# Kernel optimization log

Measured on AMD Instinct MI355X. Metric: run time of the kernel, lower is better.

Reference implementation:

```python
import jax, jax.numpy as jnp
import numpy as np

B, TE, TD, H, N_HIDDEN = 8, 4096, 1024, 256, 256

def setup_inputs() -> dict:
    key = jax.random.key(0)
    k_e, k_d, k_w, k_b = jax.random.split(key, 4)
    e = jax.random.normal(k_e, (B, TE, H), dtype=jnp.float32)
    d = jax.random.normal(k_d, (B, TD, H), dtype=jnp.float32)
    # Dense(n_hidden, activation='tanh') params: kernel [2H, n_hidden], bias [n_hidden]
    W = jax.random.normal(k_w, (2 * H, N_HIDDEN), dtype=jnp.float32) * (1.0 / np.sqrt(2 * H))
    b = jnp.zeros((N_HIDDEN,), dtype=jnp.float32)
    return {"e": e, "d": d, "W": W, "b": b}

def reference(e, d, W, b):
    # scores: Dot(axes=(2,2)) -> [B, Td, Te]
    scores = jnp.einsum('bth,bsh->bts', d, e)
    attn = jax.nn.softmax(scores, axis=-1)
    # value: Dot(axes=(2,1)) -> [B, Td, H]
    value = jnp.einsum('bts,bsh->bth', attn, e)
    concat = jnp.concatenate([value, d], axis=-1)  # [B, Td, 2H]
    return jnp.tanh(concat @ W + b)  # [B, Td, n_hidden]
```

## Files before the change

kernel.cpp:

```cpp
#include <hip/hip_runtime.h>


#define B_ 8
#define TE_ 4096
#define TD_ 1024
#define H_ 256
#define NS_ 4
#define CHUNK_ (TE_ / NS_)
#define NIT_ (CHUNK_ / 32)
#define NROW_ (B_ * TD_)

typedef __attribute__((ext_vector_type(8))) short s16x8;
typedef __attribute__((ext_vector_type(8))) _Float16 h16x8;
typedef __attribute__((ext_vector_type(4))) float fx4;
typedef __attribute__((ext_vector_type(16))) float fx16;
typedef __attribute__((ext_vector_type(4))) unsigned short u16x4;

__device__ __forceinline__ h16x8 as_h(s16x8 v) {
  union { s16x8 s; h16x8 h; } u; u.s = v; return u.h;
}
#define MFMA(a, b, c) __builtin_amdgcn_mfma_f32_16x16x32_f16(as_h(a), as_h(b), c, 0, 0, 0)
#define MFMA32(a, b, c) __builtin_amdgcn_mfma_f32_32x32x16_f16(as_h(a), as_h(b), c, 0, 0, 0)

__device__ __forceinline__ unsigned short f2h(float x) {
  const _Float16 h = (_Float16)x;
  union { _Float16 h; unsigned short s; } u; u.h = h; return u.s;
}
__device__ __forceinline__ float h2f(unsigned short s) {
  union { unsigned short s; _Float16 h; } u; u.s = s; return (float)u.h;
}
__device__ __forceinline__ unsigned pk2h(float f0, float f1) {
  return (unsigned)f2h(f0) | ((unsigned)f2h(f1) << 16);
}
__device__ __forceinline__ void gload_lds16(const void* g, void* l) {
  __builtin_amdgcn_global_load_lds(
      (const __attribute__((address_space(1))) void*)g,
      (__attribute__((address_space(3))) void*)l, 16, 0, 0);
}

__global__ __launch_bounds__(256) void prep(const float* __restrict__ e,
                                            const float* __restrict__ W,
                                            unsigned short* __restrict__ eh,
                                            unsigned short* __restrict__ eT,
                                            unsigned short* __restrict__ WT) {
  __shared__ unsigned short lt[64][65];
  __shared__ float wl[32][33];
  const int bid = blockIdx.x;
  const int tid = threadIdx.x;
  if (bid < 2048) {
    const int b = bid >> 8;
    const int s0 = ((bid >> 2) & 63) * 64;
    const int h0 = (bid & 3) * 64;
#pragma unroll
    for (int i = 0; i < 4; ++i) {
      const int row = (tid >> 4) + 16 * i;
      const int col = (tid & 15) * 4;
      const size_t go = (((size_t)b * TE_) + s0 + row) * H_ + h0 + col;
      const fx4 v = *(const fx4*)&e[go];
      u16x4 hv;
#pragma unroll
      for (int j = 0; j < 4; ++j) {
        const unsigned short hb = f2h(v[j]);
        hv[j] = hb;
        lt[row][col + j] = hb;
      }
      *(u16x4*)&eh[go] = hv;
    }
    __syncthreads();
#pragma unroll
    for (int i = 0; i < 2; ++i) {
      const int idx = tid + 256 * i;
      const int hh = idx >> 3;
      const int sc = (idx & 7) * 8;
      s16x8 v;
#pragma unroll
      for (int j = 0; j < 8; ++j) v[j] = (short)lt[sc + j][hh];
      *(s16x8*)&eT[(((size_t)b * H_) + h0 + hh) * TE_ + s0 + sc] = v;
    }
  } else {
    const int tb = bid - 2048;
    const int k0 = (tb >> 3) * 32, n0 = (tb & 7) * 32;
    const int r = tid >> 3, c4 = (tid & 7) * 4;
    const fx4 v = *(const fx4*)&W[(size_t)(k0 + r) * 256 + n0 + c4];
#pragma unroll
    for (int j = 0; j < 4; ++j) wl[r][c4 + j] = v[j];
    __syncthreads();
    u16x4 o;
#pragma unroll
    for (int j = 0; j < 4; ++j) o[j] = f2h(wl[c4 + j][r]);
    *(u16x4*)&WT[(size_t)(n0 + r) * 512 + k0 + c4] = o;
  }
}

__global__ __launch_bounds__(512, 2) void flash15(
    const unsigned short* __restrict__ eh_g, const unsigned short* __restrict__ eT_g,
    const float* __restrict__ dmat,
    unsigned short* __restrict__ pacc, float* __restrict__ pm,
    float* __restrict__ pl) {
  const int bid = blockIdx.x;
  const int ns = bid & 3;
  const int qb = (bid >> 2) & 7;
  const int b = bid >> 5;
  const int tid = threadIdx.x;
  const int w = tid >> 6;
  const int lane = tid & 63;
  const int g = lane >> 4, c = lane & 15;
  const int qrow = qb * 128 + w * 16 + c;

  __shared__ uint4 smem[2][2][1024];

  const unsigned short *peh0, *peh1, *pet0, *pet1;
  {
    const size_t ebase = ((size_t)b * TE_ + ns * CHUNK_) * H_;
    const size_t tbase = (size_t)b * H_ * TE_ + ns * CHUNK_;
    int L = tid;
    int s = L >> 5, ch = L & 31;
    int sg = (s & 3) | (((s >> 3) & 1) << 2);
    peh0 = eh_g + ebase + s * H_ + (ch ^ sg) * 8;
    int h2 = (L >> 6) * 16 + (L & 15), sc = ((L >> 4) & 3) * 8;
    pet0 = eT_g + tbase + (size_t)h2 * TE_ + sc;
    L = tid + 512;
    s = L >> 5; ch = L & 31;
    sg = (s & 3) | (((s >> 3) & 1) << 2);
    peh1 = eh_g + ebase + s * H_ + (ch ^ sg) * 8;
    h2 = (L >> 6) * 16 + (L & 15); sc = ((L >> 4) & 3) * 8;
    pet1 = eT_g + tbase + (size_t)h2 * TE_ + sc;
  }
  auto STAGE = [&](int buf) {
    uint4* ehb = smem[buf][0];
    uint4* etb = smem[buf][1];
    gload_lds16(peh0, &ehb[tid]);
    gload_lds16(peh1, &ehb[tid + 512]);
    gload_lds16(pet0, &etb[tid]);
    gload_lds16(pet1, &etb[tid + 512]);
    peh0 += 32 * H_; peh1 += 32 * H_;
    pet0 += 32; pet1 += 32;
  };

  STAGE(0);

  s16x8 bd_h[8], bd_l[8];
  {
    const float* dr = dmat + ((size_t)b * TD_ + qrow) * H_;
#pragma unroll
    for (int kk = 0; kk < 8; ++kk) {
      const fx4 x0 = *(const fx4*)&dr[kk * 32 + g * 8];
      const fx4 x1 = *(const fx4*)&dr[kk * 32 + g * 8 + 4];
      s16x8 hh, ll;
#pragma unroll
      for (int j = 0; j < 4; ++j) {
        unsigned short hb = f2h(x0[j]);
        hh[j] = (short)hb; ll[j] = (short)f2h(x0[j] - h2f(hb));
        hb = f2h(x1[j]);
        hh[4 + j] = (short)hb; ll[4 + j] = (short)f2h(x1[j] - h2f(hb));
      }
      bd_h[kk] = hh; bd_l[kk] = ll;
    }
  }

  fx4 acc[16];
#pragma unroll
  for (int nt = 0; nt < 16; ++nt) acc[nt] = (fx4){0.f, 0.f, 0.f, 0.f};
  float m = -__builtin_inff(), l = 0.f;
  const int xr = (c & 3) | (((c >> 2) & 1) << 2);
  const int rho = (c & 3) + (c >> 2) * 8;

  __syncthreads();

  for (int it = 0; it < NIT_; ++it) {
    const int cur = it & 1;
    if (it + 1 < NIT_) STAGE(cur ^ 1);

    const uint4* ehb = smem[cur][0];
    const uint4* etb = smem[cur][1];

    fx4 sa0 = (fx4){0.f, 0.f, 0.f, 0.f};
    fx4 sa1 = (fx4){0.f, 0.f, 0.f, 0.f};
#pragma unroll
    for (int kk = 0; kk < 8; ++kk) {
      const int sl = (kk * 4 + g) ^ xr;
      const s16x8 ah0 = *(const s16x8*)&ehb[rho * 32 + sl];
      const s16x8 ah1 = *(const s16x8*)&ehb[(rho + 4) * 32 + sl];
      sa0 = MFMA(ah0, bd_h[kk], sa0);
      sa0 = MFMA(ah0, bd_l[kk], sa0);
      sa1 = MFMA(ah1, bd_h[kk], sa1);
      sa1 = MFMA(ah1, bd_l[kk], sa1);
    }

    float mx = fmaxf(fmaxf(fmaxf(sa0[0], sa0[1]), fmaxf(sa0[2], sa0[3])),
                     fmaxf(fmaxf(sa1[0], sa1[1]), fmaxf(sa1[2], sa1[3])));
    mx = fmaxf(mx, __shfl_xor(mx, 16, 64));
    mx = fmaxf(mx, __shfl_xor(mx, 32, 64));
    if (!__all(mx <= m + 4.0f)) {
      const float nm = fmaxf(m, mx);
      const float sc = __expf(m - nm);
      m = nm; l *= sc;
#pragma unroll
      for (int nt = 0; nt < 16; ++nt) {
#pragma unroll
        for (int r = 0; r < 4; ++r) acc[nt][r] *= sc;
      }
    }
    float t0[4], t1[4];
    float rs = 0.f;
#pragma unroll
    for (int r = 0; r < 4; ++r) {
      t0[r] = __expf(sa0[r] - m);
      t1[r] = __expf(sa1[r] - m);
      rs += t0[r] + t1[r];
    }
    rs += __shfl_xor(rs, 16, 64);
    rs += __shfl_xor(rs, 32, 64);
    l += rs;

    union { unsigned u[4]; s16x8 v; } pb;
    pb.u[0] = pk2h(t0[0], t0[1]);
    pb.u[1] = pk2h(t0[2], t0[3]);
    pb.u[2] = pk2h(t1[0], t1[1]);
    pb.u[3] = pk2h(t1[2], t1[3]);

#pragma unroll
    for (int nt = 0; nt < 16; ++nt) {
      const s16x8 ea = *(const s16x8*)&etb[nt * 64 + g * 16 + c];
      acc[nt] = MFMA(ea, pb.v, acc[nt]);
    }
    __syncthreads();
  }

  const size_t R = (size_t)b * TD_ + qrow;
  unsigned short* pr = pacc + (((size_t)ns * NROW_) + R) * H_;
#pragma unroll
  for (int nt = 0; nt < 16; ++nt) {
    u16x4 o;
#pragma unroll
    for (int j = 0; j < 4; ++j) o[j] = f2h(acc[nt][j]);
    *(u16x4*)(pr + nt * 16 + g * 4) = o;
  }
  if (g == 0) {
    pm[ns * NROW_ + R] = m;
    pl[ns * NROW_ + R] = l;
  }
}

__global__ __launch_bounds__(256) void dense2(const unsigned short* __restrict__ pacc,
                                              const float* __restrict__ pm,
                                              const float* __restrict__ pl,
                                              const float* __restrict__ dmat,
                                              const unsigned short* __restrict__ WT,
                                              const float* __restrict__ bias,
                                              float* __restrict__ out) {
  const int row0 = blockIdx.x * 32;
  const int tid = threadIdx.x;
  const int w = tid >> 6;
  const int lane = tid & 63;
  const int ln = lane & 31, hi = lane >> 5;
  __shared__ unsigned short Xl[32][520];

  {
    const int row = tid >> 3;
    const int c0 = (tid & 7) * 32;
    const int R = row0 + row;
    float wts[NS_];
    float M = -__builtin_inff();
#pragma unroll
    for (int s = 0; s < NS_; ++s) M = fmaxf(M, pm[s * NROW_ + R]);
    float L = 0.f;
#pragma unroll
    for (int s = 0; s < NS_; ++s) {
      wts[s] = __expf(pm[s * NROW_ + R] - M);
      L += wts[s] * pl[s * NROW_ + R];
    }
    const float inv = 1.0f / L;
#pragma unroll
    for (int c8 = 0; c8 < 4; ++c8) {
      const int cc = c0 + c8 * 8;
      float o8[8];
#pragma unroll
      for (int j = 0; j < 8; ++j) o8[j] = 0.f;
#pragma unroll
      for (int s = 0; s < NS_; ++s) {
        const s16x8 v = *(const s16x8*)&pacc[(((size_t)s * NROW_) + R) * H_ + cc];
#pragma unroll
        for (int j = 0; j < 8; ++j)
          o8[j] += wts[s] * h2f((unsigned short)v[j]);
      }
      u16x4 y0, y1;
#pragma unroll
      for (int j = 0; j < 4; ++j) {
        y0[j] = f2h(o8[j] * inv);
        y1[j] = f2h(o8[4 + j] * inv);
      }
      *(u16x4*)&Xl[row][cc] = y0;
      *(u16x4*)&Xl[row][cc + 4] = y1;
    }
    const float* drow = dmat + (size_t)R * H_ + c0;
#pragma unroll
    for (int c8 = 0; c8 < 8; ++c8) {
      const fx4 v = *(const fx4*)&drow[c8 * 4];
      u16x4 y;
#pragma unroll
      for (int j = 0; j < 4; ++j) y[j] = f2h(v[j]);
      *(u16x4*)&Xl[row][256 + c0 + c8 * 4] = y;
    }
  }
  __syncthreads();

  fx16 a0, a1;
#pragma unroll
  for (int r = 0; r < 16; ++r) { a0[r] = 0.f; a1[r] = 0.f; }
  const int n0 = w * 64;
#pragma unroll
  for (int ks = 0; ks < 32; ++ks) {
    const s16x8 av = *(const s16x8*)&Xl[ln][ks * 16 + hi * 8];
    const s16x8 b0 = *(const s16x8*)(WT + (size_t)(n0 + ln) * 512 + ks * 16 + hi * 8);
    const s16x8 b1 = *(const s16x8*)(WT + (size_t)(n0 + 32 + ln) * 512 + ks * 16 + hi * 8);
    a0 = MFMA32(av, b0, a0);
    a1 = MFMA32(av, b1, a1);
  }
  const float bn0 = bias[n0 + ln];
  const float bn1 = bias[n0 + 32 + ln];
#pragma unroll
  for (int r = 0; r < 16; ++r) {
    const int rloc = (r & 3) + 8 * (r >> 2) + 4 * hi;
    const size_t ro = (size_t)(row0 + rloc) * 256;
    out[ro + n0 + ln] = tanhf(a0[r] + bn0);
    out[ro + n0 + 32 + ln] = tanhf(a1[r] + bn1);
  }
}

extern "C" void kernel_launch(void* const* d_in, const int* in_sizes, int n_in,
                              void* d_out, int out_size, void* d_ws, size_t ws_size,
                              hipStream_t stream) {
  const float* e = (const float*)d_in[0];
  const float* d = (const float*)d_in[1];
  const float* W = (const float*)d_in[2];
  const float* bias = (const float*)d_in[3];
  float* out = (float*)d_out;

  char* p = (char*)d_ws;
  const size_t EB = (size_t)B_ * TE_ * H_ * 2;
  const size_t WB = (size_t)512 * 256 * 2;
  const size_t PB = (size_t)NS_ * NROW_ * H_ * 2;
  unsigned short* eh  = (unsigned short*)p;            p += EB;
  unsigned short* eT  = (unsigned short*)p;            p += EB;
  unsigned short* WT  = (unsigned short*)p;            p += WB;
  unsigned short* pacc = (unsigned short*)p;           p += PB;
  float* pmv = (float*)p;                              p += (size_t)NS_ * NROW_ * 4;
  float* plv = (float*)p;

  prep<<<dim3(2176), dim3(256), 0, stream>>>(e, W, eh, eT, WT);
  flash15<<<dim3(256), dim3(512), 0, stream>>>(eh, eT, d, pacc, pmv, plv);
  dense2<<<dim3(256), dim3(256), 0, stream>>>(pacc, pmv, plv, d, WT, bias, out);
}
```

Baseline: 95.11 us.

## Process two key tiles per iteration with four-deep LDS buffering and deferred row-sum

New measurement: 92.67 us. 1.03x faster.

```diff
diff --git a/kernel.cpp b/kernel.cpp
--- a/kernel.cpp
+++ b/kernel.cpp
@@ -92,7 +92,7 @@
   }
 }
 
-__global__ __launch_bounds__(512, 2) void flash15(
+__global__ __launch_bounds__(512, 2) void flash16(
     const unsigned short* __restrict__ eh_g, const unsigned short* __restrict__ eT_g,
     const float* __restrict__ dmat,
     unsigned short* __restrict__ pacc, float* __restrict__ pm,
@@ -107,7 +107,7 @@
   const int g = lane >> 4, c = lane & 15;
   const int qrow = qb * 128 + w * 16 + c;
 
-  __shared__ uint4 smem[2][2][1024];
+  __shared__ uint4 smem[4][2][1024];
 
   const unsigned short *peh0, *peh1, *pet0, *pet1;
   {
@@ -138,6 +138,7 @@
   };
 
   STAGE(0);
+  STAGE(1);
 
   s16x8 bd_h[8], bd_l[8];
   {
@@ -161,71 +162,106 @@
   fx4 acc[16];
 #pragma unroll
   for (int nt = 0; nt < 16; ++nt) acc[nt] = (fx4){0.f, 0.f, 0.f, 0.f};
-  float m = -__builtin_inff(), l = 0.f;
+  float m = -__builtin_inff(), l_lane = 0.f;
   const int xr = (c & 3) | (((c >> 2) & 1) << 2);
   const int rho = (c & 3) + (c >> 2) * 8;
 
   __syncthreads();
 
-  for (int it = 0; it < NIT_; ++it) {
-    const int cur = it & 1;
-    if (it + 1 < NIT_) STAGE(cur ^ 1);
-
-    const uint4* ehb = smem[cur][0];
-    const uint4* etb = smem[cur][1];
-
-    fx4 sa0 = (fx4){0.f, 0.f, 0.f, 0.f};
-    fx4 sa1 = (fx4){0.f, 0.f, 0.f, 0.f};
+  for (int p = 0; p < NIT_ / 2; ++p) {
+    const int bufA = (p & 1) << 1;
+    const int bufB = bufA + 1;
+    if (p + 1 < NIT_ / 2) {
+      STAGE(bufA ^ 2);
+      STAGE(bufB ^ 2);
+    }
+    const uint4* ehbA = smem[bufA][0];
+    const uint4* etbA = smem[bufA][1];
+    const uint4* ehbB = smem[bufB][0];
+    const uint4* etbB = smem[bufB][1];
+
+    fx4 sA0 = (fx4){0.f, 0.f, 0.f, 0.f};
+    fx4 sA1 = (fx4){0.f, 0.f, 0.f, 0.f};
+    fx4 sB0 = (fx4){0.f, 0.f, 0.f, 0.f};
+    fx4 sB1 = (fx4){0.f, 0.f, 0.f, 0.f};
 #pragma unroll
     for (int kk = 0; kk < 8; ++kk) {
       const int sl = (kk * 4 + g) ^ xr;
-      const s16x8 ah0 = *(const s16x8*)&ehb[rho * 32 + sl];
-      const s16x8 ah1 = *(const s16x8*)&ehb[(rho + 4) * 32 + sl];
-      sa0 = MFMA(ah0, bd_h[kk], sa0);
-      sa0 = MFMA(ah0, bd_l[kk], sa0);
-      sa1 = MFMA(ah1, bd_h[kk], sa1);
-      sa1 = MFMA(ah1, bd_l[kk], sa1);
-    }
-
-    float mx = fmaxf(fmaxf(fmaxf(sa0[0], sa0[1]), fmaxf(sa0[2], sa0[3])),
-                     fmaxf(fmaxf(sa1[0], sa1[1]), fmaxf(sa1[2], sa1[3])));
+      const s16x8 aA0 = *(const s16x8*)&ehbA[rho * 32 + sl];
+      const s16x8 aA1 = *(const s16x8*)&ehbA[(rho + 4) * 32 + sl];
+      const s16x8 aB0 = *(const s16x8*)&ehbB[rho * 32 + sl];
+      const s16x8 aB1 = *(const s16x8*)&ehbB[(rho + 4) * 32 + sl];
+      sA0 = MFMA(aA0, bd_h[kk], sA0);
+      sA0 = MFMA(aA0, bd_l[kk], sA0);
+      sA1 = MFMA(aA1, bd_h[kk], sA1);
+      sA1 = MFMA(aA1, bd_l[kk], sA1);
+      sB0 = MFMA(aB0, bd_h[kk], sB0);
+      sB0 = MFMA(aB0, bd_l[kk], sB0);
+      sB1 = MFMA(aB1, bd_h[kk], sB1);
+      sB1 = MFMA(aB1, bd_l[kk], sB1);
+    }
+
+    float mx = fmaxf(fmaxf(fmaxf(sA0[0], sA0[1]), fmaxf(sA0[2], sA0[3])),
+                     fmaxf(fmaxf(sA1[0], sA1[1]), fmaxf(sA1[2], sA1[3])));
+    mx = fmaxf(mx, fmaxf(fmaxf(fmaxf(sB0[0], sB0[1]), fmaxf(sB0[2], sB0[3])),
+                         fmaxf(fmaxf(sB1[0], sB1[1]), fmaxf(sB1[2], sB1[3]))));
     mx = fmaxf(mx, __shfl_xor(mx, 16, 64));
     mx = fmaxf(mx, __shfl_xor(mx, 32, 64));
     if (!__all(mx <= m + 4.0f)) {
       const float nm = fmaxf(m, mx);
       const float sc = __expf(m - nm);
-      m = nm; l *= sc;
+      m = nm; l_lane *= sc;
 #pragma unroll
       for (int nt = 0; nt < 16; ++nt) {
 #pragma unroll
         for (int r = 0; r < 4; ++r) acc[nt][r] *= sc;
       }
     }
-    float t0[4], t1[4];
-    float rs = 0.f;
-#pragma unroll
-    for (int r = 0; r < 4; ++r) {
-      t0[r] = __expf(sa0[r] - m);
-      t1[r] = __expf(sa1[r] - m);
-      rs += t0[r] + t1[r];
-    }
-    rs += __shfl_xor(rs, 16, 64);
-    rs += __shfl_xor(rs, 32, 64);
-    l += rs;
-
-    union { unsigned u[4]; s16x8 v; } pb;
-    pb.u[0] = pk2h(t0[0], t0[1]);
-    pb.u[1] = pk2h(t0[2], t0[3]);
-    pb.u[2] = pk2h(t1[0], t1[1]);
-    pb.u[3] = pk2h(t1[2], t1[3]);
-
-#pragma unroll
-    for (int nt = 0; nt < 16; ++nt) {
-      const s16x8 ea = *(const s16x8*)&etb[nt * 64 + g * 16 + c];
-      acc[nt] = MFMA(ea, pb.v, acc[nt]);
+
+    {
+      float t0[4], t1[4];
+#pragma unroll
+      for (int r = 0; r < 4; ++r) {
+        t0[r] = __expf(sA0[r] - m);
+        t1[r] = __expf(sA1[r] - m);
+        l_lane += t0[r] + t1[r];
+      }
+      union { unsigned u[4]; s16x8 v; } pb;
+      pb.u[0] = pk2h(t0[0], t0[1]);
+      pb.u[1] = pk2h(t0[2], t0[3]);
+      pb.u[2] = pk2h(t1[0], t1[1]);
+      pb.u[3] = pk2h(t1[2], t1[3]);
+#pragma unroll
+      for (int nt = 0; nt < 16; ++nt) {
+        const s16x8 ea = *(const s16x8*)&etbA[nt * 64 + g * 16 + c];
+        acc[nt] = MFMA(ea, pb.v, acc[nt]);
+      }
+    }
+    {
+      float t0[4], t1[4];
+#pragma unroll
+      for (int r = 0; r < 4; ++r) {
+        t0[r] = __expf(sB0[r] - m);
+        t1[r] = __expf(sB1[r] - m);
+        l_lane += t0[r] + t1[r];
+      }
+      union { unsigned u[4]; s16x8 v; } pb;
+      pb.u[0] = pk2h(t0[0], t0[1]);
+      pb.u[1] = pk2h(t0[2], t0[3]);
+      pb.u[2] = pk2h(t1[0], t1[1]);
+      pb.u[3] = pk2h(t1[2], t1[3]);
+#pragma unroll
+      for (int nt = 0; nt < 16; ++nt) {
+        const s16x8 ea = *(const s16x8*)&etbB[nt * 64 + g * 16 + c];
+        acc[nt] = MFMA(ea, pb.v, acc[nt]);
+      }
     }
     __syncthreads();
   }
+
+  float l = l_lane;
+  l += __shfl_xor(l, 16, 64);
+  l += __shfl_xor(l, 32, 64);
 
   const size_t R = (size_t)b * TD_ + qrow;
   unsigned short* pr = pacc + (((size_t)ns * NROW_) + R) * H_;
@@ -349,6 +385,6 @@
   float* plv = (float*)p;
 
   prep<<<dim3(2176), dim3(256), 0, stream>>>(e, W, eh, eT, WT);
-  flash15<<<dim3(256), dim3(512), 0, stream>>>(eh, eT, d, pacc, pmv, plv);
+  flash16<<<dim3(256), dim3(512), 0, stream>>>(eh, eT, d, pacc, pmv, plv);
   dense2<<<dim3(256), dim3(256), 0, stream>>>(pacc, pmv, plv, d, WT, bias, out);
 }
```
